# Kernel optimization log

Hardware: AMD Instinct MI355X
Metric: run time of the kernel (lower is better)

## Reference

```python
import math
import jax, jax.numpy as jnp
import numpy as np

DIM = 2048
NUM_HEADS = 32
NUM_KV_HEADS = 8
HEAD_DIM = DIM // NUM_HEADS
KV_REPEAT = NUM_HEADS // NUM_KV_HEADS
BSZ, SEQ = 2, 2048
THRESHOLD = 0.05


def ternarize_ste(w):
    # scale = mean(|w|), clamped; ternary in {-1,0,1}; STE: fwd value is ternary,
    # grad flows straight through to w.
    scale = jnp.maximum(jnp.abs(w).mean(), 1e-6)
    ternary = jnp.where(w > THRESHOLD * scale, 1.0,
                        jnp.where(w < -THRESHOLD * scale, -1.0, 0.0)).astype(w.dtype)
    return w + jax.lax.stop_gradient(ternary - w)


def setup_inputs() -> dict:
    key = jax.random.key(0)
    kx, kq, kk, kv, ko = jax.random.split(key, 5)
    # kaiming_uniform_(a=sqrt(5)) => U(-b, b) with b = 1/sqrt(in_features)
    bound = 1.0 / math.sqrt(DIM)
    return {
        "x": jax.random.normal(kx, (BSZ, SEQ, DIM), dtype=jnp.float32),
        "wq": jax.random.uniform(kq, (DIM, DIM), jnp.float32, -bound, bound),
        "wk": jax.random.uniform(kk, (HEAD_DIM * NUM_KV_HEADS, DIM), jnp.float32, -bound, bound),
        "wv": jax.random.uniform(kv, (HEAD_DIM * NUM_KV_HEADS, DIM), jnp.float32, -bound, bound),
        "wo": jax.random.uniform(ko, (DIM, DIM), jnp.float32, -bound, bound),
    }


def reference(x, wq, wk, wv, wo):
    bsz, seq, _ = x.shape
    # BitLinear projections with ternarized weights (F.linear: x @ W^T)
    q = x @ ternarize_ste(wq).T                      # [b, s, dim]
    k = x @ ternarize_ste(wk).T                      # [b, s, kvh*hd]
    v = x @ ternarize_ste(wv).T

    q = q.reshape(bsz, seq, NUM_HEADS, HEAD_DIM)     # [b, s, H, d]
    k = k.reshape(bsz, seq, NUM_KV_HEADS, HEAD_DIM)
    v = v.reshape(bsz, seq, NUM_KV_HEADS, HEAD_DIM)
    # repeat_interleave over the kv-head axis to match query heads
    k = jnp.repeat(k, KV_REPEAT, axis=2)             # [b, s, H, d]
    v = jnp.repeat(v, KV_REPEAT, axis=2)

    scale = 1.0 / math.sqrt(HEAD_DIM)
    att = jnp.einsum('bqhd,bkhd->bhqk', q, k) * scale  # [b, H, s, s]
    causal = jnp.tril(jnp.ones((seq, seq), dtype=bool))
    att = jnp.where(causal, att, -jnp.inf)
    probs = jax.nn.softmax(att, axis=-1)
    out = jnp.einsum('bhqk,bkhd->bqhd', probs, v).reshape(bsz, seq, DIM)
    return out @ ternarize_ste(wo).T
```

## Files before the change

### kernel.cpp

```cpp
#include <hip/hip_runtime.h>

typedef _Float16 f16;
typedef f16  f16x8 __attribute__((ext_vector_type(8)));
typedef f16  f16x4 __attribute__((ext_vector_type(4)));
typedef float f32x4 __attribute__((ext_vector_type(4)));

#define DIM_   2048
#define SEQ_   2048
#define BATCH_ 2
#define MROWS_ (BATCH_*SEQ_)
#define HD_    64
#define KVW_   512

__device__ __forceinline__ f32x4 mfma16(f16x8 a, f16x8 b, f32x4 c) {
  return __builtin_amdgcn_mfma_f32_16x16x32_f16(a, b, c, 0, 0, 0);
}

typedef const __attribute__((address_space(1))) void gas_void;
typedef __attribute__((address_space(3))) void las_void;
__device__ __forceinline__ void gload16(const void* g, void* l) {
  __builtin_amdgcn_global_load_lds((gas_void*)g, (las_void*)l, 16, 0, 0);
}

__device__ __forceinline__ unsigned long long pk4(float a, float b, float c, float d) {
  union { _Float16 h[4]; unsigned long long u; } z;
  auto p0 = __builtin_amdgcn_cvt_pkrtz(a, b);
  auto p1 = __builtin_amdgcn_cvt_pkrtz(c, d);
  z.h[0] = p0[0]; z.h[1] = p0[1]; z.h[2] = p1[0]; z.h[3] = p1[1];
  return z.u;
}

__global__ __launch_bounds__(256)
void prep1(const float* __restrict__ x,
           const float* __restrict__ w0, const float* __restrict__ w1,
           const float* __restrict__ w2, const float* __restrict__ w3,
           float* __restrict__ parts, f16* __restrict__ hi, f16* __restrict__ lo) {
  const int id = blockIdx.y;
  if (id < 4) {
    const float* w = id == 0 ? w0 : id == 1 ? w1 : id == 2 ? w2 : w3;
    const int n4 = (id == 1 || id == 2) ? (KVW_ * DIM_ / 4) : (DIM_ * DIM_ / 4);
    float s = 0.f;
    for (int i = blockIdx.x * 256 + threadIdx.x; i < n4; i += gridDim.x * 256) {
      float4 v = *(const float4*)(w + (long)i * 4);
      s += fabsf(v.x) + fabsf(v.y) + fabsf(v.z) + fabsf(v.w);
    }
    #pragma unroll
    for (int off = 32; off > 0; off >>= 1)
      s += __shfl_down(s, off, 64);
    __shared__ float red[4];
    int lane = threadIdx.x & 63, wv = threadIdx.x >> 6;
    if (lane == 0) red[wv] = s;
    __syncthreads();
    if (threadIdx.x == 0)
      parts[id * 192 + blockIdx.x] = (red[0] + red[1]) + (red[2] + red[3]);
  } else {
    const int half = (MROWS_ * DIM_ / 4) / 2;
    const long base = (long)(id - 4) * half;
    for (int i = blockIdx.x * 256 + threadIdx.x; i < half; i += gridDim.x * 256) {
      float4 v = *(const float4*)(x + (base + i) * 4);
      f16x4 h, l;
      h[0] = (f16)v.x; l[0] = (f16)(v.x - (float)h[0]);
      h[1] = (f16)v.y; l[1] = (f16)(v.y - (float)h[1]);
      h[2] = (f16)v.z; l[2] = (f16)(v.z - (float)h[2]);
      h[3] = (f16)v.w; l[3] = (f16)(v.w - (float)h[3]);
      *(f16x4*)(hi + (base + i) * 4) = h;
      *(f16x4*)(lo + (base + i) * 4) = l;
    }
  }
}

__global__ __launch_bounds__(256)
void ternarize4(const float* __restrict__ w0, const float* __restrict__ w1,
                const float* __restrict__ w2, const float* __restrict__ w3,
                unsigned short* __restrict__ t0, unsigned short* __restrict__ t1,
                unsigned short* __restrict__ t2, unsigned short* __restrict__ t3,
                const float* __restrict__ parts) {
  const int id = blockIdx.y;
  const float* w = id == 0 ? w0 : id == 1 ? w1 : id == 2 ? w2 : w3;
  unsigned short* t = id == 0 ? t0 : id == 1 ? t1 : id == 2 ? t2 : t3;
  const int n = (id == 1 || id == 2) ? (KVW_ * DIM_) : (DIM_ * DIM_);

  __shared__ float thr_s;
  if (threadIdx.x < 64) {
    const int lane = threadIdx.x;
    float s = parts[id * 192 + lane] + parts[id * 192 + 64 + lane]
            + parts[id * 192 + 128 + lane];
    #pragma unroll
    for (int off = 32; off > 0; off >>= 1)
      s += __shfl_down(s, off, 64);
    if (lane == 0) thr_s = 0.05f * fmaxf(s / (float)n, 1e-6f);
  }
  __syncthreads();
  const float thr = thr_s;

  const int n4 = n >> 2;
  for (int i = blockIdx.x * 256 + threadIdx.x; i < n4; i += gridDim.x * 256) {
    float4 v = *(const float4*)(w + (long)i * 4);
    ushort4 o;
    o.x = v.x > thr ? 0x3C00 : (v.x < -thr ? 0xBC00 : 0);
    o.y = v.y > thr ? 0x3C00 : (v.y < -thr ? 0xBC00 : 0);
    o.z = v.z > thr ? 0x3C00 : (v.z < -thr ? 0xBC00 : 0);
    o.w = v.w > thr ? 0x3C00 : (v.w < -thr ? 0xBC00 : 0);
    *(ushort4*)(t + (long)i * 4) = o;
  }
}

__global__ __launch_bounds__(256, 2)
void gemm_qkv(const f16* __restrict__ Ah, const f16* __restrict__ Al,
              const f16* __restrict__ Bw,
              f16* __restrict__ O1, f16* __restrict__ O2,
              f16* __restrict__ K1, f16* __restrict__ K2,
              f16* __restrict__ OV) {
  constexpr int BUFSZ = 32768;
  __shared__ __attribute__((aligned(16))) char smem[2 * BUFSZ];

  const int id2 = (blockIdx.x & 7) * 48 + (blockIdx.x >> 3);
  const int bx  = id2 % 12;
  const int by  = id2 / 12;
  const int brow = by * 128;
  const int bcol = bx * 256;

  const int tid  = threadIdx.x;
  const int lane = tid & 63;
  const int wv   = tid >> 6;
  const int wr   = (wv >> 1) * 64;
  const int wc   = (wv & 1) * 128;
  const int fr   = lane & 15;
  const int fq   = lane >> 4;

  const bool lo_on = bcol < 2560;

  const int rl  = lane >> 2;
  const int scg = ((lane & 3) ^ ((lane >> 3) & 3)) * 8;
  const f16* gA0 = Ah + (long)(brow + wv * 32 + rl) * DIM_ + scg;
  const f16* gL0 = Al + (long)(brow + wv * 32 + rl) * DIM_ + scg;
  const f16* gB0 = Bw + (long)(bcol + wv * 64 + rl) * DIM_ + scg;
  const int wvbA = __builtin_amdgcn_readfirstlane(wv * 1024);
  const int wvbB = __builtin_amdgcn_readfirstlane(wv * 2048);

  auto STAGE = [&](int kt, int buf) {
    const int k0 = kt * 32;
    char* base = smem + buf * BUFSZ;
    f16* lA = (f16*)base + wvbA;
    f16* lL = (f16*)(base + 8192) + wvbA;
    f16* lB = (f16*)(base + 16384) + wvbB;
    gload16(gA0 + k0, lA);
    gload16(gA0 + k0 + 16 * DIM_, lA + 512);
    gload16(gB0 + k0, lB);
    gload16(gB0 + k0 + 16 * DIM_, lB + 512);
    gload16(gB0 + k0 + 32 * DIM_, lB + 1024);
    gload16(gB0 + k0 + 48 * DIM_, lB + 1536);
    if (lo_on) {
      gload16(gL0 + k0, lL);
      gload16(gL0 + k0 + 16 * DIM_, lL + 512);
    }
  };

  const int xga = (fq ^ ((fr >> 1) & 3)) * 8;

  f32x4 acc[4][8] = {};
  const int nk = DIM_ / 32;

  STAGE(0, 0);
  #pragma unroll 1
  for (int kt = 0; kt < nk; ++kt) {
    asm volatile("s_waitcnt vmcnt(0)" ::: "memory");
    __syncthreads();
    if (kt + 1 < nk) STAGE(kt + 1, (kt + 1) & 1);

    const char* base = smem + (kt & 1) * BUFSZ;
    const f16* cAh = (const f16*)base;
    const f16* cAl = (const f16*)(base + 8192);
    const f16* cB  = (const f16*)(base + 16384);

    f16x8 bfr[8];
    #pragma unroll
    for (int ni = 0; ni < 8; ++ni)
      bfr[ni] = *(const f16x8*)(cB + (wc + ni * 16 + fr) * 32 + xga);
    #pragma unroll
    for (int mi = 0; mi < 4; ++mi) {
      const int aoff = (wr + mi * 16 + fr) * 32 + xga;
      f16x8 ah = *(const f16x8*)(cAh + aoff);
      #pragma unroll
      for (int ni = 0; ni < 8; ++ni)
        acc[mi][ni] = mfma16(ah, bfr[ni], acc[mi][ni]);
      if (lo_on) {
        f16x8 al = *(const f16x8*)(cAl + aoff);
        #pragma unroll
        for (int ni = 0; ni < 8; ++ni)
          acc[mi][ni] = mfma16(al, bfr[ni], acc[mi][ni]);
      }
    }
  }

  const int colbase = bcol + wc;
  if (colbase < 2048) {
    #pragma unroll
    for (int mi = 0; mi < 4; ++mi)
      #pragma unroll
      for (int ni = 0; ni < 8; ++ni)
        #pragma unroll
        for (int r = 0; r < 4; ++r) {
          long idx = (long)(brow + wr + mi * 16 + fq * 4 + r) * DIM_
                   + colbase + ni * 16 + fr;
          float v = acc[mi][ni][r];
          f16 hv = (f16)v;
          O1[idx] = hv;
          O2[idx] = (f16)(v - (float)hv);
        }
  } else if (colbase < 2560) {
    #pragma unroll
    for (int mi = 0; mi < 4; ++mi)
      #pragma unroll
      for (int ni = 0; ni < 8; ++ni)
        #pragma unroll
        for (int r = 0; r < 4; ++r) {
          long idx = (long)(brow + wr + mi * 16 + fq * 4 + r) * KVW_
                   + (colbase - 2048) + ni * 16 + fr;
          float v = acc[mi][ni][r];
          f16 hv = (f16)v;
          K1[idx] = hv;
          K2[idx] = (f16)(v - (float)hv);
        }
  } else {
    f16* st = (f16*)smem + wv * 32 * 72;
    const int bb = brow >> 11;
    const int s0 = (brow & (SEQ_ - 1)) + wr;
    #pragma unroll
    for (int nh = 0; nh < 4; ++nh) {
      const int khh = ((colbase - 2560) >> 6) + (nh >> 1);
      const int db  = (nh & 1) * 32;
      #pragma unroll
      for (int nj = 0; nj < 2; ++nj) {
        const int ni = nh * 2 + nj;
        #pragma unroll
        for (int mi = 0; mi < 4; ++mi)
          #pragma unroll
          for (int r = 0; r < 4; ++r)
            st[(nj * 16 + fr) * 72 + mi * 16 + fq * 4 + r] = (f16)acc[mi][ni][r];
      }
      #pragma unroll
      for (int i = 0; i < 4; ++i) {
        int dl = i * 8 + (lane >> 3);
        f16x8 v = *(const f16x8*)(st + dl * 72 + (lane & 7) * 8);
        *(f16x8*)(OV + ((long)(bb * 8 + khh) * 64 + db + dl) * SEQ_
                  + s0 + (lane & 7) * 8) = v;
      }
    }
  }
}

__global__ __launch_bounds__(256)
void gemm_o(const f16* __restrict__ A, const f16* __restrict__ Bw,
            float* __restrict__ C) {
  constexpr int BUFSZ = 16384;
  __shared__ __attribute__((aligned(16))) char smem[2 * BUFSZ];

  const int cpx = gridDim.x >> 3;
  const int id2 = (blockIdx.x & 7) * cpx + (blockIdx.x >> 3);
  const int nbx = DIM_ >> 7;
  const int bx  = id2 % nbx;
  const int by  = id2 / nbx;
  const int brow = by * 128;
  const int bcol = bx * 128;

  const int tid  = threadIdx.x;
  const int lane = tid & 63;
  const int wv   = tid >> 6;
  const int wr   = (wv >> 1) * 64;
  const int wc   = (wv & 1) * 64;
  const int fr   = lane & 15;
  const int fq   = lane >> 4;

  const int srw = wv * 32 + (lane >> 2);
  const int scg = ((lane & 3) ^ ((lane >> 3) & 3)) * 8;
  const f16* gA0 = A + (long)(brow + srw) * DIM_ + scg;
  const f16* gA1 = gA0 + 16 * (long)DIM_;
  const f16* gB0 = Bw + (long)(bcol + srw) * DIM_ + scg;
  const f16* gB1 = gB0 + 16 * (long)DIM_;
  const int wvb = __builtin_amdgcn_readfirstlane(wv * 1024);

  auto STAGE = [&](int kt, int buf) {
    const int k0 = kt * 32;
    char* base = smem + buf * BUFSZ;
    f16* lA = (f16*)base + wvb;
    f16* lB = (f16*)(base + 8192) + wvb;
    gload16(gA0 + k0, lA);
    gload16(gA1 + k0, lA + 512);
    gload16(gB0 + k0, lB);
    gload16(gB1 + k0, lB + 512);
  };

  const int xga = (fq ^ ((fr >> 1) & 3)) * 8;

  f32x4 acc[4][4] = {};
  const int nk = DIM_ >> 5;

  STAGE(0, 0);
  #pragma unroll 1
  for (int kt = 0; kt < nk; ++kt) {
    asm volatile("s_waitcnt vmcnt(0)" ::: "memory");
    __syncthreads();
    if (kt + 1 < nk) STAGE(kt + 1, (kt + 1) & 1);

    const char* base = smem + (kt & 1) * BUFSZ;
    const f16* cA = (const f16*)base;
    const f16* cB = (const f16*)(base + 8192);

    f16x8 bfr[4];
    #pragma unroll
    for (int ni = 0; ni < 4; ++ni)
      bfr[ni] = *(const f16x8*)(cB + (wc + ni * 16 + fr) * 32 + xga);
    #pragma unroll
    for (int mi = 0; mi < 4; ++mi) {
      f16x8 ah = *(const f16x8*)(cA + (wr + mi * 16 + fr) * 32 + xga);
      #pragma unroll
      for (int ni = 0; ni < 4; ++ni)
        acc[mi][ni] = mfma16(ah, bfr[ni], acc[mi][ni]);
    }
  }

  #pragma unroll
  for (int mi = 0; mi < 4; ++mi)
    #pragma unroll
    for (int ni = 0; ni < 4; ++ni)
      #pragma unroll
      for (int r = 0; r < 4; ++r)
        C[(long)(brow + wr + mi * 16 + fq * 4 + r) * DIM_ + (bcol + wc + ni * 16 + fr)]
            = acc[mi][ni][r];
}

__global__ __launch_bounds__(256, 3)
void attn_kernel(const f16* __restrict__ qhi, const f16* __restrict__ qlo,
                 const f16* __restrict__ khi, const f16* __restrict__ klo,
                 const f16* __restrict__ vt,  f16* __restrict__ AO) {
  const int id2   = (blockIdx.x & 7) * 128 + (blockIdx.x >> 3);
  const int local = id2 & 127;
  const int t     = 63 - (local >> 1);
  const int cmb   = (id2 >> 7) * 2 + (local & 1);
  const int kh    = cmb & 7;
  const int b     = cmb >> 3;
  const int tid  = threadIdx.x;
  const int lane = tid & 63;
  const int w    = tid >> 6;
  const int fr   = lane & 15;
  const int fq   = lane >> 4;
  const int h    = kh * 4 + w;
  const int xr   = (fr & 7) << 4;

  __shared__ __attribute__((aligned(16))) char sKh[64 * 128];
  __shared__ __attribute__((aligned(16))) char sKl[64 * 128];
  __shared__ __attribute__((aligned(16))) char sVt[2][64 * 128];
  __shared__ __attribute__((aligned(16))) char sP [4][2][16 * 128];

  const int srow = w * 16 + (lane >> 3);
  const int scol = ((lane & 7) ^ (lane >> 3)) * 8;
  const f16* gK0 = khi + ((long)(b * SEQ_) + srow) * KVW_ + kh * HD_ + scol;
  const f16* gL0 = klo + ((long)(b * SEQ_) + srow) * KVW_ + kh * HD_ + scol;
  const f16* gV0 = vt + ((long)(b * 8 + kh) * HD_ + srow) * SEQ_ + scol;
  const int ldso = __builtin_amdgcn_readfirstlane(w * 2048);

  auto STAGE_K = [&](int kb) {
    const long ko = (long)kb * 64 * KVW_;
    gload16(gK0 + ko,            sKh + ldso);
    gload16(gK0 + ko + 8 * KVW_, sKh + ldso + 1024);
    gload16(gL0 + ko,            sKl + ldso);
    gload16(gL0 + ko + 8 * KVW_, sKl + ldso + 1024);
  };
  auto STAGE_V = [&](int kb, int buf) {
    const long vo = (long)kb * 64;
    gload16(gV0 + vo,            (char*)sVt[buf] + ldso);
    gload16(gV0 + vo + 8 * SEQ_, (char*)sVt[buf] + ldso + 1024);
  };

  char* pw0 = sP[w][0];
  char* pw1 = sP[w][1];
  const float ce = 0.125f * 1.44269504f;

  const int nkv   = (t >> 1) + 1;
  const int qrow0 = t * 32;

  f16x8 qh[2][2], ql[2][2];
  #pragma unroll
  for (int st = 0; st < 2; ++st)
    #pragma unroll
    for (int ks = 0; ks < 2; ++ks) {
      const long qoff = (long)(b * SEQ_ + qrow0 + st * 16 + fr) * DIM_
                      + h * HD_ + ks * 32 + fq * 8;
      qh[st][ks] = *(const f16x8*)(qhi + qoff);
      ql[st][ks] = *(const f16x8*)(qlo + qoff);
    }

  STAGE_K(0);
  STAGE_V(0, 0);

  float m0 = -1e30f, m1 = -1e30f, l0 = 0.f, l1 = 0.f;
  f32x4 o0[4] = {}, o1[4] = {};

  #pragma unroll 1
  for (int kb = 0; kb < nkv; ++kb) {
    asm volatile("s_waitcnt vmcnt(0)" ::: "memory");
    __syncthreads();
    if (kb + 1 < nkv) STAGE_V(kb + 1, (kb + 1) & 1);
    const char* bV = sVt[kb & 1];

    f32x4 s0[4] = {}, s1[4] = {};
    __builtin_amdgcn_s_setprio(1);
    #pragma unroll
    for (int ks = 0; ks < 2; ++ks)
      #pragma unroll
      for (int ni = 0; ni < 4; ++ni) {
        const int rb = (ni * 16 + fr) * 128 + ((ks * 64 + fq * 16) ^ xr);
        f16x8 ah = *(const f16x8*)(sKh + rb);
        f16x8 af = *(const f16x8*)(sKl + rb);
        s0[ni] = mfma16(ah, qh[0][ks], s0[ni]);
        s0[ni] = mfma16(ah, ql[0][ks], s0[ni]);
        s0[ni] = mfma16(af, qh[0][ks], s0[ni]);
        s1[ni] = mfma16(ah, qh[1][ks], s1[ni]);
        s1[ni] = mfma16(ah, ql[1][ks], s1[ni]);
        s1[ni] = mfma16(af, qh[1][ks], s1[ni]);
      }
    __builtin_amdgcn_s_setprio(0);

    __syncthreads();
    if (kb + 1 < nkv) STAGE_K(kb + 1);

    if (kb == nkv - 1) {
      #pragma unroll
      for (int ni = 0; ni < 4; ++ni)
        #pragma unroll
        for (int r = 0; r < 4; ++r) {
          const int kk = ni * 16 + fq * 4 + r;
          if (kk > (t & 1) * 32 + fr)      s0[ni][r] = -1e30f;
          if (kk > (t & 1) * 32 + 16 + fr) s1[ni][r] = -1e30f;
        }
    }

    #pragma unroll
    for (int st = 0; st < 2; ++st) {
      f32x4* s = st ? s1 : s0;
      float& m = st ? m1 : m0;
      float& l = st ? l1 : l0;
      f32x4* o = st ? o1 : o0;
      char* pw = st ? pw1 : pw0;

      float ma = fmaxf(fmaxf(s[0][0], s[0][1]), fmaxf(s[0][2], s[0][3]));
      float mb2 = fmaxf(fmaxf(s[1][0], s[1][1]), fmaxf(s[1][2], s[1][3]));
      float mc = fmaxf(fmaxf(s[2][0], s[2][1]), fmaxf(s[2][2], s[2][3]));
      float md = fmaxf(fmaxf(s[3][0], s[3][1]), fmaxf(s[3][2], s[3][3]));
      float mb = fmaxf(fmaxf(ma, mb2), fmaxf(mc, md));
      mb = fmaxf(mb, __shfl_xor(mb, 16, 64));
      mb = fmaxf(mb, __shfl_xor(mb, 32, 64));

      const float mo = m;
      const bool trig = mb > mo + 64.f;
      const float mn = trig ? mb : mo;
      m = mn;
      const float al = exp2f((mo - mn) * ce);
      const float tt = mn * ce;

      float rs = 0.f;
      #pragma unroll
      for (int ni = 0; ni < 4; ++ni) {
        #pragma unroll
        for (int r = 0; r < 4; ++r) {
          float pv = exp2f(fmaf(s[ni][r], ce, -tt));
          s[ni][r] = pv;
          rs += pv;
        }
        *(unsigned long long*)(pw + ((fr * 128 + ni * 32 + fq * 8) ^ xr)) =
            pk4(s[ni][0], s[ni][1], s[ni][2], s[ni][3]);
      }
      rs += __shfl_xor(rs, 16, 64);
      rs += __shfl_xor(rs, 32, 64);
      l = l * al + rs;

      if (__any(trig)) {
        #pragma unroll
        for (int r = 0; r < 4; ++r) {
          float alr = __shfl(al, ((lane >> 4) << 2) + r, 64);
          o[0][r] *= alr; o[1][r] *= alr; o[2][r] *= alr; o[3][r] *= alr;
        }
      }
    }

    __builtin_amdgcn_s_setprio(1);
    #pragma unroll
    for (int ks = 0; ks < 2; ++ks) {
      const int pb = (fr * 128 + ks * 64 + fq * 16) ^ xr;
      f16x8 pa0 = *(const f16x8*)(pw0 + pb);
      f16x8 pa1 = *(const f16x8*)(pw1 + pb);
      #pragma unroll
      for (int di = 0; di < 4; ++di) {
        f16x8 vf = *(const f16x8*)(bV + (di * 16 + fr) * 128
                                   + ((ks * 64 + fq * 16) ^ xr));
        o0[di] = mfma16(pa0, vf, o0[di]);
        o1[di] = mfma16(pa1, vf, o1[di]);
      }
    }
    __builtin_amdgcn_s_setprio(0);
  }

  #pragma unroll
  for (int st = 0; st < 2; ++st) {
    const f32x4* o = st ? o1 : o0;
    const float l = st ? l1 : l0;
    float linv[4];
    #pragma unroll
    for (int r = 0; r < 4; ++r)
      linv[r] = 1.f / __shfl(l, ((lane >> 4) << 2) + r, 64);
    #pragma unroll
    for (int di = 0; di < 4; ++di)
      #pragma unroll
      for (int r = 0; r < 4; ++r)
        AO[(long)(b * SEQ_ + qrow0 + st * 16 + fq * 4 + r) * DIM_
           + h * HD_ + di * 16 + fr] = (f16)(o[di][r] * linv[r]);
  }
}

extern "C" void kernel_launch(void* const* d_in, const int* in_sizes, int n_in,
                              void* d_out, int out_size, void* d_ws, size_t ws_size,
                              hipStream_t stream) {
  const float* x  = (const float*)d_in[0];
  const float* wq = (const float*)d_in[1];
  const float* wk = (const float*)d_in[2];
  const float* wv = (const float*)d_in[3];
  const float* wo = (const float*)d_in[4];
  char* ws = (char*)d_ws;

  size_t off = 0;
  float* parts = (float*)ws;                off = 4096;
  f16* x_hi  = (f16*)(ws + off);            off += (size_t)MROWS_ * DIM_ * 2;
  f16* x_lo  = (f16*)(ws + off);            off += (size_t)MROWS_ * DIM_ * 2;
  f16* wq_t  = (f16*)(ws + off);            off += (size_t)DIM_ * DIM_ * 2;
  f16* wkv_t = (f16*)(ws + off);            off += (size_t)1024 * DIM_ * 2;
  f16* wo_t  = (f16*)(ws + off);            off += (size_t)DIM_ * DIM_ * 2;
  f16* qhi   = (f16*)(ws + off);            off += (size_t)MROWS_ * DIM_ * 2;
  f16* qlo   = (f16*)(ws + off);            off += (size_t)MROWS_ * DIM_ * 2;
  f16* khi   = (f16*)(ws + off);            off += (size_t)MROWS_ * KVW_ * 2;
  f16* klo   = (f16*)(ws + off);            off += (size_t)MROWS_ * KVW_ * 2;
  f16* vtb   = (f16*)(ws + off);            off += (size_t)BATCH_ * 8 * 64 * SEQ_ * 2;
  f16* ao    = (f16*)(ws + off);            off += (size_t)MROWS_ * DIM_ * 2;

  prep1<<<dim3(192, 6), dim3(256), 0, stream>>>(x, wq, wk, wv, wo,
                                                parts, x_hi, x_lo);
  ternarize4<<<dim3(192, 4), dim3(256), 0, stream>>>(
      wq, wk, wv, wo,
      (unsigned short*)wq_t, (unsigned short*)wkv_t,
      (unsigned short*)(wkv_t + (size_t)KVW_ * DIM_), (unsigned short*)wo_t,
      parts);

  gemm_qkv<<<dim3(384), dim3(256), 0, stream>>>(
      x_hi, x_lo, wq_t, qhi, qlo, khi, klo, vtb);

  attn_kernel<<<dim3(1024), dim3(256), 0, stream>>>(
      qhi, qlo, khi, klo, vtb, ao);

  gemm_o<<<dim3((DIM_ / 128) * (MROWS_ / 128)), dim3(256), 0, stream>>>(
      ao, wo_t, (float*)d_out);
}
```

Before: 271.8 us.

## Shrink QKV GEMM block tile to 128x128 with two waves per block

Changes the QKV projection GEMM from 256-thread blocks computing 128x256 tiles to 128-thread blocks computing 128x128 tiles, with each of two waves owning 64 rows and all 128 columns. The grid doubles to 768 blocks and LDS per buffer drops, with the staging loads reorganised so each wave loads four row groups per operand. The aim is more blocks for better load balance across CUs and lower LDS per block. The cost is less B-tile reuse per block and more global traffic for A.

```diff
diff --git a/kernel.cpp b/kernel.cpp
--- a/kernel.cpp
+++ b/kernel.cpp
@@ -105,26 +105,25 @@
   }
 }
 
-__global__ __launch_bounds__(256, 2)
+__global__ __launch_bounds__(128, 2)
 void gemm_qkv(const f16* __restrict__ Ah, const f16* __restrict__ Al,
               const f16* __restrict__ Bw,
               f16* __restrict__ O1, f16* __restrict__ O2,
               f16* __restrict__ K1, f16* __restrict__ K2,
               f16* __restrict__ OV) {
-  constexpr int BUFSZ = 32768;
+  constexpr int BUFSZ = 24576;
   __shared__ __attribute__((aligned(16))) char smem[2 * BUFSZ];
 
-  const int id2 = (blockIdx.x & 7) * 48 + (blockIdx.x >> 3);
-  const int bx  = id2 % 12;
-  const int by  = id2 / 12;
+  const int id2 = (blockIdx.x & 7) * 96 + (blockIdx.x >> 3);
+  const int bx  = id2 % 24;
+  const int by  = id2 / 24;
   const int brow = by * 128;
-  const int bcol = bx * 256;
+  const int bcol = bx * 128;
 
   const int tid  = threadIdx.x;
   const int lane = tid & 63;
   const int wv   = tid >> 6;
-  const int wr   = (wv >> 1) * 64;
-  const int wc   = (wv & 1) * 128;
+  const int wr   = wv * 64;
   const int fr   = lane & 15;
   const int fq   = lane >> 4;
 
@@ -132,27 +131,26 @@
 
   const int rl  = lane >> 2;
   const int scg = ((lane & 3) ^ ((lane >> 3) & 3)) * 8;
-  const f16* gA0 = Ah + (long)(brow + wv * 32 + rl) * DIM_ + scg;
-  const f16* gL0 = Al + (long)(brow + wv * 32 + rl) * DIM_ + scg;
+  const f16* gA0 = Ah + (long)(brow + wv * 64 + rl) * DIM_ + scg;
+  const f16* gL0 = Al + (long)(brow + wv * 64 + rl) * DIM_ + scg;
   const f16* gB0 = Bw + (long)(bcol + wv * 64 + rl) * DIM_ + scg;
-  const int wvbA = __builtin_amdgcn_readfirstlane(wv * 1024);
-  const int wvbB = __builtin_amdgcn_readfirstlane(wv * 2048);
+  const int wvb = __builtin_amdgcn_readfirstlane(wv * 2048);
 
   auto STAGE = [&](int kt, int buf) {
     const int k0 = kt * 32;
     char* base = smem + buf * BUFSZ;
-    f16* lA = (f16*)base + wvbA;
-    f16* lL = (f16*)(base + 8192) + wvbA;
-    f16* lB = (f16*)(base + 16384) + wvbB;
-    gload16(gA0 + k0, lA);
-    gload16(gA0 + k0 + 16 * DIM_, lA + 512);
-    gload16(gB0 + k0, lB);
-    gload16(gB0 + k0 + 16 * DIM_, lB + 512);
-    gload16(gB0 + k0 + 32 * DIM_, lB + 1024);
-    gload16(gB0 + k0 + 48 * DIM_, lB + 1536);
+    f16* lA = (f16*)base + wvb;
+    f16* lL = (f16*)(base + 8192) + wvb;
+    f16* lB = (f16*)(base + 16384) + wvb;
+    #pragma unroll
+    for (int g = 0; g < 4; ++g) {
+      gload16(gA0 + k0 + g * 16 * DIM_, lA + g * 512);
+      gload16(gB0 + k0 + g * 16 * DIM_, lB + g * 512);
+    }
     if (lo_on) {
-      gload16(gL0 + k0, lL);
-      gload16(gL0 + k0 + 16 * DIM_, lL + 512);
+      #pragma unroll
+      for (int g = 0; g < 4; ++g)
+        gload16(gL0 + k0 + g * 16 * DIM_, lL + g * 512);
     }
   };
 
@@ -176,7 +174,7 @@
     f16x8 bfr[8];
     #pragma unroll
     for (int ni = 0; ni < 8; ++ni)
-      bfr[ni] = *(const f16x8*)(cB + (wc + ni * 16 + fr) * 32 + xga);
+      bfr[ni] = *(const f16x8*)(cB + (ni * 16 + fr) * 32 + xga);
     #pragma unroll
     for (int mi = 0; mi < 4; ++mi) {
       const int aoff = (wr + mi * 16 + fr) * 32 + xga;
@@ -193,7 +191,7 @@
     }
   }
 
-  const int colbase = bcol + wc;
+  const int colbase = bcol;
   if (colbase < 2048) {
     #pragma unroll
     for (int mi = 0; mi < 4; ++mi)
@@ -550,7 +548,7 @@
       (unsigned short*)(wkv_t + (size_t)KVW_ * DIM_), (unsigned short*)wo_t,
       parts);
 
-  gemm_qkv<<<dim3(384), dim3(256), 0, stream>>>(
+  gemm_qkv<<<dim3(768), dim3(128), 0, stream>>>(
       x_hi, x_lo, wq_t, qhi, qlo, khi, klo, vtb);
 
   attn_kernel<<<dim3(1024), dim3(256), 0, stream>>>(
```

New measurement: 277.0 us. No clear change (+1.9%).
